# Kernel tuning notes

Measured on AMD Instinct MI355X. Metric: run time of the kernel, lower is better.

Reference implementation:

```python
import jax, jax.numpy as jnp
import numpy as np

EPS = 1e-5

def _ln(x, g, b):
    mu = x.mean(-1, keepdims=True)
    var = ((x - mu) ** 2).mean(-1, keepdims=True)
    return (x - mu) * jax.lax.rsqrt(var + EPS) * g + b

def setup_inputs() -> dict:
    B, K, D, H, T = 64, 64, 128, 128, 4
    key = jax.random.key(0)
    ks = jax.random.split(key, 20)
    s = 0.02
    inp = {
        "slots": jax.random.normal(ks[0], (B, K, D), jnp.float32),
        "edge_probs": jax.random.uniform(ks[1], (B, K, K), jnp.float32),
        "edge_types": jax.random.uniform(ks[2], (B, K, K, T), jnp.float32),
        # f_self: LayerNorm(D) -> Linear(D,H) -> ReLU -> Linear(H,D)
        "ls_g": jnp.ones((D,), jnp.float32),
        "ls_b": jnp.zeros((D,), jnp.float32),
        "ws1": jax.random.normal(ks[3], (D, H), jnp.float32) * s,
        "bs1": jnp.zeros((H,), jnp.float32),
        "ws2": jax.random.normal(ks[4], (H, D), jnp.float32) * s,
        "bs2": jnp.zeros((D,), jnp.float32),
        # f_inter[tau]: Linear(2D,H) -> ReLU -> Linear(H,H) -> ReLU -> Linear(H,D), stacked over T
        "wi1": jax.random.normal(ks[5], (T, 2 * D, H), jnp.float32) * s,
        "bi1": jnp.zeros((T, H), jnp.float32),
        "wi2": jax.random.normal(ks[6], (T, H, H), jnp.float32) * s,
        "bi2": jnp.zeros((T, H), jnp.float32),
        "wi3": jax.random.normal(ks[7], (T, H, D), jnp.float32) * s,
        "bi3": jnp.zeros((T, D), jnp.float32),
        # update_mlp: LayerNorm(2D) -> Linear(2D,H) -> ReLU -> Linear(H,D)
        "lu_g": jnp.ones((2 * D,), jnp.float32),
        "lu_b": jnp.zeros((2 * D,), jnp.float32),
        "wu1": jax.random.normal(ks[8], (2 * D, H), jnp.float32) * s,
        "bu1": jnp.zeros((H,), jnp.float32),
        "wu2": jax.random.normal(ks[9], (H, D), jnp.float32) * s,
        "bu2": jnp.zeros((D,), jnp.float32),
    }
    return inp

NUM_MP = 2

def reference(slots, edge_probs, edge_types, ls_g, ls_b, ws1, bs1, ws2, bs2,
              wi1, bi1, wi2, bi2, wi3, bi3, lu_g, lu_b, wu1, bu1, wu2, bu2):
    B, K, D = slots.shape
    T = edge_types.shape[-1]
    h = slots
    for _ in range(NUM_MP):
        # f_self
        delta_self = jax.nn.relu(_ln(h, ls_g, ls_b) @ ws1 + bs1) @ ws2 + bs2
        # all-pairs features: cat[b,i,j] = [h[b,i] (sender), h[b,j] (receiver)]
        sender = jnp.broadcast_to(h[:, :, None, :], (B, K, K, D))
        receiver = jnp.broadcast_to(h[:, None, :, :], (B, K, K, D))
        pair = jnp.concatenate([sender, receiver], axis=-1)  # [B,K,K,2D]
        delta_inter = jnp.zeros_like(h)
        for tau in range(T):
            x = jax.nn.relu(pair @ wi1[tau] + bi1[tau])
            x = jax.nn.relu(x @ wi2[tau] + bi2[tau])
            eff = x @ wi3[tau] + bi3[tau]  # [B,K,K,D]
            w = edge_probs[..., None] * edge_types[..., tau, None]  # [B,K,K,1]
            delta_inter = delta_inter + (eff * w).sum(axis=1)  # sum over sender i
        combined = jnp.concatenate([h + delta_self, delta_inter], axis=-1)
        update = jax.nn.relu(_ln(combined, lu_g, lu_b) @ wu1 + bu1) @ wu2 + bu2
        h = h + update  # residual=True
    return h
```

## Files before the change

### kernel.cpp

```cpp
#include <hip/hip_runtime.h>
#include <hip/hip_fp16.h>

#define BATCH 64
#define KSLOT 64
#define DDIM  128
#define HDIM  128
#define TTYPE 4
#define NSLOT (BATCH*KSLOT)
#define EPSLN 1e-5f
#define YROW  544

typedef _Float16 v8h __attribute__((ext_vector_type(8)));
typedef _Float16 v4h __attribute__((ext_vector_type(4)));
typedef _Float16 v2h __attribute__((ext_vector_type(2)));
typedef __fp16   v2y __attribute__((ext_vector_type(2)));
typedef float    v4f __attribute__((ext_vector_type(4)));

__device__ __forceinline__ float waveAllSum(float v) {
    #pragma unroll
    for (int m = 1; m < 64; m <<= 1) v += __shfl_xor(v, m, 64);
    return v;
}

__global__ __launch_bounds__(256) void k_wconv(
        const float* __restrict__ ws1, const float* __restrict__ wi1,
        const float* __restrict__ ws2, const float* __restrict__ wu1,
        const float* __restrict__ wu2, const float* __restrict__ wi3,
        const float* __restrict__ wi2, const float* __restrict__ bi1,
        const float* __restrict__ bi3,
        const float* __restrict__ ep, const float* __restrict__ et,
        __half* __restrict__ ws1T, __half* __restrict__ wi1catT,
        __half* __restrict__ ws2T, __half* __restrict__ wu1T,
        __half* __restrict__ wu2T, __half* __restrict__ w3catT,
        __half* __restrict__ w2T16, float* __restrict__ biascat,
        __half* __restrict__ wPre) {
    __shared__ __align__(16) float tile[128*132];
    int bx = blockIdx.x, tid = threadIdx.x;
    if (bx >= 22) {
        int bx2 = bx - 22, tau = bx2 & 3, b = bx2 >> 2;
        const float* epb = ep + (size_t)b*4096;
        const float* etb = et + (size_t)b*4096*TTYPE + tau;
        __half* dst = wPre + ((size_t)tau*BATCH + b)*4096;
        for (int idx = tid; idx < 4096; idx += 256)
            dst[idx] = __float2half(epb[idx] * etb[(size_t)idx*TTYPE]);
        return;
    }
    if (bx == 21) {
        for (int idx = tid; idx < 128*32; idx += 256) {
            int o = idx >> 5, c = idx & 31;
            w3catT[(size_t)o*YROW + 512 + c] = (c < 4) ? __float2half(bi3[c*DDIM + o]) : __float2half(0.f);
        }
        for (int idx = tid; idx < 1024; idx += 256) {
            int th = idx >> 7, o = idx & 127;
            biascat[idx] = (th & 1) ? bi1[(th>>1)*HDIM + o] : 0.f;
        }
        return;
    }
    const float* src; __half* dst; int dstride = 128, dcol = 0;
    if (bx == 0)      { src = ws1; dst = ws1T; }
    else if (bx <= 8) { int th = bx-1, tau = th>>1, half = th&1;
                        src = wi1 + ((size_t)tau*256 + half*128)*128;
                        dst = wi1catT + (size_t)th*128*128; }
    else if (bx == 9) { src = ws2; dst = ws2T; }
    else if (bx ==10) { src = wu2; dst = wu2T; }
    else if (bx <=12) { int hh = bx-11; src = wu1 + (size_t)hh*128*128;
                        dst = wu1T; dstride = 256; dcol = hh*128; }
    else if (bx <=16) { int tau = bx-13; src = wi3 + (size_t)tau*16384;
                        dst = w3catT; dstride = YROW; dcol = tau*128; }
    else              { int tau = bx-17; src = wi2 + (size_t)tau*16384;
                        dst = w2T16 + (size_t)tau*16384; }
    for (int idx = tid; idx < 4096; idx += 256) {
        int r = idx >> 5, c4 = idx & 31;
        *(float4*)&tile[r*132 + c4*4] = *(const float4*)&src[(size_t)r*128 + c4*4];
    }
    __syncthreads();
    for (int idx = tid; idx < 8192; idx += 256) {
        int n = idx >> 6, kp = idx & 63;
        __half2 p = __floats2half2_rn(tile[(2*kp)*132 + n], tile[(2*kp+1)*132 + n]);
        *(__half2*)&dst[(size_t)n*dstride + dcol + 2*kp] = p;
    }
}

__global__ __launch_bounds__(256) void k_front(
        const float* __restrict__ h,
        const __half* __restrict__ wi1catT, const float* __restrict__ biascat,
        const float* __restrict__ ls_g, const float* __restrict__ ls_b,
        const __half* __restrict__ ws1T, const float* __restrict__ bs1,
        const __half* __restrict__ ws2T, const float* __restrict__ bs2,
        __half* __restrict__ AtCt, float* __restrict__ comb128) {
    __shared__ __align__(16) char smem[17152];
    int tid = threadIdx.x, lane = tid & 63, w = tid >> 6;
    int n = lane & 15, quad = lane >> 4;
    int row0 = blockIdx.x*16, nb = blockIdx.y;
    if (nb < 4) {
        _Float16* Ha = (_Float16*)smem;
        v8h bfrag[4][4];
        #pragma unroll
        for (int ot = 0; ot < 4; ot++) {
            int col = nb*256 + w*64 + ot*16 + n;
            #pragma unroll
            for (int ks = 0; ks < 4; ks++)
                bfrag[ot][ks] = *(const v8h*)&wi1catT[(size_t)col*128 + ks*32 + quad*8];
        }
        for (int u = tid; u < 16*32; u += 256) {
            int r = u >> 5, c4 = (u & 31)*4;
            float4 f = *(const float4*)&h[(size_t)(row0 + r)*128 + c4];
            *(__half2*)&Ha[r*136 + c4]     = __floats2half2_rn(f.x, f.y);
            *(__half2*)&Ha[r*136 + c4 + 2] = __floats2half2_rn(f.z, f.w);
        }
        __syncthreads();
        v4f acc[4];
        #pragma unroll
        for (int ot = 0; ot < 4; ot++) {
            float b0 = biascat[nb*256 + w*64 + ot*16 + n];
            acc[ot] = (v4f){b0, b0, b0, b0};
        }
        #pragma unroll
        for (int ks = 0; ks < 4; ks++) {
            v8h a = *(const v8h*)&Ha[n*136 + ks*32 + quad*8];
            #pragma unroll
            for (int ot = 0; ot < 4; ot++)
                acc[ot] = __builtin_amdgcn_mfma_f32_16x16x32_f16(a, bfrag[ot][ks], acc[ot], 0, 0, 0);
        }
        __syncthreads();
        _Float16* Ot = (_Float16*)smem;
        #pragma unroll
        for (int ot = 0; ot < 4; ot++)
            #pragma unroll
            for (int r = 0; r < 4; r++)
                Ot[(quad*4 + r)*264 + w*64 + ot*16 + n] = (_Float16)acc[ot][r];
        __syncthreads();
        #pragma unroll
        for (int u = 0; u < 2; u++) {
            int k = tid + u*256;
            int r = k >> 5, c8 = (k & 31)*8;
            *(v8h*)&AtCt[(size_t)(row0 + r)*1024 + nb*256 + c8] = *(const v8h*)&Ot[r*264 + c8];
        }
    } else {
        float*    Hrow = (float*)smem;
        _Float16* Xa = (_Float16*)(smem + 8448);
        _Float16* Tt = (_Float16*)(smem + 8448 + 4352);
        v8h b1[2][4], b2[2][4];
        #pragma unroll
        for (int ot = 0; ot < 2; ot++) {
            int col = w*32 + ot*16 + n;
            #pragma unroll
            for (int ks = 0; ks < 4; ks++) {
                b1[ot][ks] = *(const v8h*)&ws1T[(size_t)col*128 + ks*32 + quad*8];
                b2[ot][ks] = *(const v8h*)&ws2T[(size_t)col*128 + ks*32 + quad*8];
            }
        }
        for (int u = tid; u < 16*32; u += 256) {
            int r = u >> 5, c4 = (u & 31)*4;
            *(float4*)&Hrow[r*132 + c4] = *(const float4*)&h[(size_t)(row0 + r)*128 + c4];
        }
        __syncthreads();
        #pragma unroll
        for (int rr = 0; rr < 4; rr++) {
            int r = w*4 + rr;
            float x0 = Hrow[r*132 + 2*lane], x1 = Hrow[r*132 + 2*lane + 1];
            float mu = waveAllSum(x0 + x1) * (1.f/128.f);
            float d0 = x0 - mu, d1 = x1 - mu;
            float var = waveAllSum(d0*d0 + d1*d1) * (1.f/128.f);
            float rs = rsqrtf(var + EPSLN);
            float2 gv = *(const float2*)&ls_g[2*lane];
            float2 bv = *(const float2*)&ls_b[2*lane];
            *(__half2*)&Xa[r*136 + 2*lane] = __floats2half2_rn(d0*rs*gv.x + bv.x, d1*rs*gv.y + bv.y);
        }
        __syncthreads();
        v4f acc[2];
        #pragma unroll
        for (int ot = 0; ot < 2; ot++) { float b0 = bs1[w*32 + ot*16 + n]; acc[ot] = (v4f){b0,b0,b0,b0}; }
        #pragma unroll
        for (int ks = 0; ks < 4; ks++) {
            v8h a = *(const v8h*)&Xa[n*136 + ks*32 + quad*8];
            #pragma unroll
            for (int ot = 0; ot < 2; ot++)
                acc[ot] = __builtin_amdgcn_mfma_f32_16x16x32_f16(a, b1[ot][ks], acc[ot], 0, 0, 0);
        }
        #pragma unroll
        for (int ot = 0; ot < 2; ot++)
            #pragma unroll
            for (int r = 0; r < 4; r++)
                Tt[(quad*4 + r)*136 + w*32 + ot*16 + n] = (_Float16)fmaxf(acc[ot][r], 0.f);
        __syncthreads();
        #pragma unroll
        for (int ot = 0; ot < 2; ot++) { float b0 = bs2[w*32 + ot*16 + n]; acc[ot] = (v4f){b0,b0,b0,b0}; }
        #pragma unroll
        for (int ks = 0; ks < 4; ks++) {
            v8h a = *(const v8h*)&Tt[n*136 + ks*32 + quad*8];
            #pragma unroll
            for (int ot = 0; ot < 2; ot++)
                acc[ot] = __builtin_amdgcn_mfma_f32_16x16x32_f16(a, b2[ot][ks], acc[ot], 0, 0, 0);
        }
        #pragma unroll
        for (int ot = 0; ot < 2; ot++)
            #pragma unroll
            for (int r = 0; r < 4; r++) {
                int rr = quad*4 + r, col = w*32 + ot*16 + n;
                comb128[(size_t)(row0 + rr)*128 + col] = Hrow[rr*132 + col] + acc[ot][r];
            }
    }
}

#define LROW 136
__global__ __launch_bounds__(512) void k_pair(
        const __half* __restrict__ AtCt,
        const __half* __restrict__ w2T16,
        const float* __restrict__ bi2,
        const __half* __restrict__ wPre,
        __half* __restrict__ Ycat) {
    __shared__ __align__(16) _Float16 w2T[HDIM*LROW];
    __shared__ __align__(16) _Float16 Cs[KSLOT*LROW];
    __shared__ __align__(16) _Float16 As[KSLOT*LROW];
    __shared__ __align__(16) _Float16 wS[KSLOT*KSLOT];
    int bx = blockIdx.x, b = bx >> 2, tau = bx & 3;
    int tid = threadIdx.x, lane = tid & 63, w = tid >> 6;
    int jt = w >> 1, oh = w & 1, quad = lane >> 4, n = lane & 15;

    for (int idx = tid; idx < 2048; idx += 512) {
        int o = idx >> 4, seg = (idx & 15)*8;
        *(v8h*)&w2T[o*LROW + seg] = *(const v8h*)&w2T16[((size_t)tau*128 + o)*128 + seg];
    }
    for (int u = tid; u < 1024; u += 512) {
        int j = u >> 4, seg = (u & 15)*8;
        const __half* rp = AtCt + (size_t)(b*KSLOT + j)*1024 + tau*256 + seg;
        *(v8h*)&As[j*LROW + seg] = *(const v8h*)&rp[0];
        *(v8h*)&Cs[j*LROW + seg] = *(const v8h*)&rp[128];
    }
    {
        const __half* wsrc = wPre + ((size_t)tau*BATCH + b)*4096;
        int base = tid*8;
        *(v8h*)&wS[base] = *(const v8h*)&wsrc[base];
    }
    __syncthreads();

    v8h bfrag[4][4];
    #pragma unroll
    for (int ot = 0; ot < 4; ot++)
        #pragma unroll
        for (int ks = 0; ks < 4; ks++)
            bfrag[ot][ks] = *(const v8h*)&w2T[(oh*64 + ot*16 + n)*LROW + ks*32 + quad*8];
    v8h cfrag[4];
    #pragma unroll
    for (int ks = 0; ks < 4; ks++)
        cfrag[ks] = *(const v8h*)&Cs[(jt*16 + n)*LROW + ks*32 + quad*8];
    v4f biasvec[4];
    #pragma unroll
    for (int ot = 0; ot < 4; ot++) {
        float b0 = bi2[tau*HDIM + oh*64 + ot*16 + n];
        biasvec[ot] = (v4f){b0, b0, b0, b0};
    }

    v4h yacch[4];
    #pragma unroll
    for (int ot = 0; ot < 4; ot++) yacch[ot] = (v4h){0,0,0,0};
    v4h wsacch = (v4h){0,0,0,0};
    const v8h zero8 = {0,0,0,0,0,0,0,0};
    const v4h zero4h = {0,0,0,0};

    v8h aN[4]; v4h wvN;
    #pragma unroll
    for (int ks = 0; ks < 4; ks++) aN[ks] = *(const v8h*)&As[ks*32 + quad*8];
    wvN = *(const v4h*)&wS[jt*16 + quad*4];

    for (int i = 0; i < KSLOT; ++i) {
        v8h a[4]; v4h wv = wvN;
        #pragma unroll
        for (int ks = 0; ks < 4; ks++) a[ks] = aN[ks];
        if (i < KSLOT-1) {
            #pragma unroll
            for (int ks = 0; ks < 4; ks++)
                aN[ks] = *(const v8h*)&As[(i+1)*LROW + ks*32 + quad*8];
            wvN = *(const v4h*)&wS[(i+1)*KSLOT + jt*16 + quad*4];
        }
        v8h x1[4];
        #pragma unroll
        for (int ks = 0; ks < 4; ks++)
            x1[ks] = __builtin_elementwise_max(a[ks] + cfrag[ks], zero8);
        #pragma unroll
        for (int ot = 0; ot < 4; ot++) {
            v4f acc = __builtin_amdgcn_mfma_f32_16x16x32_f16(x1[0], bfrag[ot][0], biasvec[ot], 0, 0, 0);
            #pragma unroll
            for (int ks = 1; ks < 4; ks++)
                acc = __builtin_amdgcn_mfma_f32_16x16x32_f16(x1[ks], bfrag[ot][ks], acc, 0, 0, 0);
            v2h lo = __builtin_bit_cast(v2h, __builtin_amdgcn_cvt_pkrtz(acc[0], acc[1]));
            v2h hi = __builtin_bit_cast(v2h, __builtin_amdgcn_cvt_pkrtz(acc[2], acc[3]));
            v4h rel = {lo[0], lo[1], hi[0], hi[1]};
            rel = __builtin_elementwise_max(rel, zero4h);
            yacch[ot] = yacch[ot] + wv * rel;
        }
        wsacch = wsacch + wv;
    }

    #pragma unroll
    for (int r = 0; r < 4; r++) {
        int j = jt*16 + quad*4 + r;
        __half* yb = Ycat + (size_t)(b*KSLOT + j)*YROW + tau*128 + oh*64;
        #pragma unroll
        for (int ot = 0; ot < 4; ot++)
            yb[ot*16 + n] = __float2half((float)yacch[ot][r]);
    }
    if (oh == 0 && n == 0) {
        #pragma unroll
        for (int r = 0; r < 4; r++)
            Ycat[(size_t)(b*KSLOT + jt*16 + quad*4 + r)*YROW + 512 + tau] = __float2half((float)wsacch[r]);
    }
}

__global__ __launch_bounds__(512, 2) void k_mega(
        const __half* __restrict__ Ycat, const __half* __restrict__ w3catT,
        const float* __restrict__ comb128,
        const float* __restrict__ g, const float* __restrict__ bb,
        const __half* __restrict__ wu1T, const float* __restrict__ bu1,
        const __half* __restrict__ wu2T, const float* __restrict__ bu2,
        const float* __restrict__ h, float* __restrict__ hout) {
    __shared__ __align__(16) _Float16 Ys[16*552];
    __shared__ __align__(16) float    Crow[16*260];
    __shared__ __align__(16) _Float16 Xa[16*264];
    __shared__ __align__(16) _Float16 Ut[16*136];
    int tid = threadIdx.x, lane = tid & 63, w = tid >> 6;
    int n = lane & 15, quad = lane >> 4;
    int row0 = blockIdx.x*16;
    v8h f3[17];
    #pragma unroll
    for (int ks = 0; ks < 17; ks++)
        f3[ks] = *(const v8h*)&w3catT[(size_t)(w*16 + n)*YROW + ks*32 + quad*8];
    v8h f1[8];
    #pragma unroll
    for (int ks = 0; ks < 8; ks++)
        f1[ks] = *(const v8h*)&wu1T[(size_t)(w*16 + n)*256 + ks*32 + quad*8];
    v8h f2[4];
    #pragma unroll
    for (int ks = 0; ks < 4; ks++)
        f2[ks] = *(const v8h*)&wu2T[(size_t)(w*16 + n)*128 + ks*32 + quad*8];

    for (int u = tid; u < 1024; u += 512) {
        int r = u >> 6, seg = (u & 63)*8;
        *(v8h*)&Ys[r*552 + seg] = *(const v8h*)&Ycat[(size_t)(row0 + r)*YROW + seg];
    }
    if (tid < 64) {
        int r = tid >> 2, seg = 512 + (tid & 3)*8;
        *(v8h*)&Ys[r*552 + seg] = *(const v8h*)&Ycat[(size_t)(row0 + r)*YROW + seg];
    }
    {
        int r = tid >> 5, c4 = (tid & 31)*4;
        *(float4*)&Crow[r*260 + c4] = *(const float4*)&comb128[(size_t)(row0 + r)*128 + c4];
    }
    __syncthreads();
    {
        v4f acc = (v4f){0.f,0.f,0.f,0.f};
        #pragma unroll
        for (int ks = 0; ks < 17; ks++) {
            v8h a = *(const v8h*)&Ys[n*552 + ks*32 + quad*8];
            acc = __builtin_amdgcn_mfma_f32_16x16x32_f16(a, f3[ks], acc, 0, 0, 0);
        }
        #pragma unroll
        for (int r = 0; r < 4; r++)
            Crow[(quad*4 + r)*260 + 128 + w*16 + n] = acc[r];
    }
    __syncthreads();
    #pragma unroll
    for (int rr = 0; rr < 2; rr++) {
        int r = w*2 + rr;
        float4 v = *(const float4*)&Crow[r*260 + 4*lane];
        float mu = waveAllSum(v.x + v.y + v.z + v.w) * (1.f/256.f);
        float d0 = v.x-mu, d1 = v.y-mu, d2 = v.z-mu, d3 = v.w-mu;
        float var = waveAllSum(d0*d0 + d1*d1 + d2*d2 + d3*d3) * (1.f/256.f);
        float rs = rsqrtf(var + EPSLN);
        float4 gv = *(const float4*)&g[4*lane];
        float4 bv = *(const float4*)&bb[4*lane];
        *(__half2*)&Xa[r*264 + 4*lane]     = __floats2half2_rn(d0*rs*gv.x + bv.x, d1*rs*gv.y + bv.y);
        *(__half2*)&Xa[r*264 + 4*lane + 2] = __floats2half2_rn(d2*rs*gv.z + bv.z, d3*rs*gv.w + bv.w);
    }
    __syncthreads();
    {
        float b0 = bu1[w*16 + n];
        v4f acc = (v4f){b0, b0, b0, b0};
        #pragma unroll
        for (int ks = 0; ks < 8; ks++) {
            v8h a = *(const v8h*)&Xa[n*264 + ks*32 + quad*8];
            acc = __builtin_amdgcn_mfma_f32_16x16x32_f16(a, f1[ks], acc, 0, 0, 0);
        }
        #pragma unroll
        for (int r = 0; r < 4; r++)
            Ut[(quad*4 + r)*136 + w*16 + n] = (_Float16)fmaxf(acc[r], 0.f);
    }
    __syncthreads();
    {
        float b0 = bu2[w*16 + n];
        v4f acc = (v4f){b0, b0, b0, b0};
        #pragma unroll
        for (int ks = 0; ks < 4; ks++) {
            v8h a = *(const v8h*)&Ut[n*136 + ks*32 + quad*8];
            acc = __builtin_amdgcn_mfma_f32_16x16x32_f16(a, f2[ks], acc, 0, 0, 0);
        }
        #pragma unroll
        for (int r = 0; r < 4; r++) {
            int rr = quad*4 + r, col = w*16 + n;
            hout[(size_t)(row0 + rr)*128 + col] = h[(size_t)(row0 + rr)*128 + col] + acc[r];
        }
    }
}

extern "C" void kernel_launch(void* const* d_in, const int* in_sizes, int n_in,
                              void* d_out, int out_size, void* d_ws, size_t ws_size,
                              hipStream_t stream) {
    const float* slots = (const float*)d_in[0];
    const float* ep    = (const float*)d_in[1];
    const float* et    = (const float*)d_in[2];
    const float* ls_g  = (const float*)d_in[3];
    const float* ls_b  = (const float*)d_in[4];
    const float* ws1   = (const float*)d_in[5];
    const float* bs1   = (const float*)d_in[6];
    const float* ws2   = (const float*)d_in[7];
    const float* bs2   = (const float*)d_in[8];
    const float* wi1   = (const float*)d_in[9];
    const float* bi1   = (const float*)d_in[10];
    const float* wi2   = (const float*)d_in[11];
    const float* bi2   = (const float*)d_in[12];
    const float* wi3   = (const float*)d_in[13];
    const float* bi3   = (const float*)d_in[14];
    const float* lu_g  = (const float*)d_in[15];
    const float* lu_b  = (const float*)d_in[16];
    const float* wu1   = (const float*)d_in[17];
    const float* bu1   = (const float*)d_in[18];
    const float* wu2   = (const float*)d_in[19];
    const float* bu2   = (const float*)d_in[20];
    float* out = (float*)d_out;

    char* p = (char*)d_ws;
    float*  h_buf   = (float*)p;   p += (size_t)NSLOT*DDIM*4;
    __half* AtCt    = (__half*)p;  p += (size_t)NSLOT*1024*2;
    __half* Ycat    = (__half*)p;  p += (size_t)NSLOT*YROW*2;
    float*  comb128 = (float*)p;   p += (size_t)NSLOT*128*4;
    __half* wPre    = (__half*)p;  p += (size_t)TTYPE*BATCH*4096*2;
    __half* ws1T    = (__half*)p;  p += 128*128*2;
    __half* wi1catT = (__half*)p;  p += 1024*128*2;
    __half* ws2T    = (__half*)p;  p += 128*128*2;
    __half* wu1T    = (__half*)p;  p += 128*256*2;
    __half* wu2T    = (__half*)p;  p += 128*128*2;
    __half* w3catT  = (__half*)p;  p += 128*YROW*2;
    __half* w2T16   = (__half*)p;  p += 4*128*128*2;
    float*  biascat = (float*)p;   p += 1024*4;

    k_wconv<<<22 + 256, 256, 0, stream>>>(ws1, wi1, ws2, wu1, wu2, wi3, wi2, bi1, bi3,
                                          ep, et, ws1T, wi1catT, ws2T, wu1T, wu2T,
                                          w3catT, w2T16, biascat, wPre);

    for (int mp = 0; mp < 2; mp++) {
        const float* h = (mp == 0) ? slots : h_buf;
        float* hout = (mp == 0) ? h_buf : out;
        k_front<<<dim3(256, 5), 256, 0, stream>>>(h, wi1catT, biascat, ls_g, ls_b,
                                                  ws1T, bs1, ws2T, bs2, AtCt, comb128);
        k_pair<<<BATCH*TTYPE, 512, 0, stream>>>(AtCt, w2T16, bi2, wPre, Ycat);
        k_mega<<<NSLOT/16, 512, 0, stream>>>(Ycat, w3catT, comb128, lu_g, lu_b,
                                             wu1T, bu1, wu2T, bu2, h, hout);
    }
}
```

Baseline: 219.6 us.

## Fuse first interaction-layer GEMM into pair kernel, drop AtCt intermediate

Moves the per-type sender/receiver projection (h @ wi1 halves) out of the front kernel and computes it inside k_pair from h loaded directly into shared memory. This removes the 16 MB fp16 AtCt global write and read round trip. The self-MLP becomes its own kernel, k_self. In exchange k_pair gains an extra GEMM stage, 17 KB more shared memory, and B-fragments read straight from global memory, which may lower occupancy and lengthen the critical path.

```diff
diff --git a/kernel.cpp b/kernel.cpp
--- a/kernel.cpp
+++ b/kernel.cpp
@@ -13,7 +13,6 @@
 typedef _Float16 v8h __attribute__((ext_vector_type(8)));
 typedef _Float16 v4h __attribute__((ext_vector_type(4)));
 typedef _Float16 v2h __attribute__((ext_vector_type(2)));
-typedef __fp16   v2y __attribute__((ext_vector_type(2)));
 typedef float    v4f __attribute__((ext_vector_type(4)));
 
 __device__ __forceinline__ float waveAllSum(float v) {
@@ -81,131 +80,85 @@
     }
 }
 
-__global__ __launch_bounds__(256) void k_front(
+__global__ __launch_bounds__(256) void k_self(
         const float* __restrict__ h,
-        const __half* __restrict__ wi1catT, const float* __restrict__ biascat,
         const float* __restrict__ ls_g, const float* __restrict__ ls_b,
         const __half* __restrict__ ws1T, const float* __restrict__ bs1,
         const __half* __restrict__ ws2T, const float* __restrict__ bs2,
-        __half* __restrict__ AtCt, float* __restrict__ comb128) {
-    __shared__ __align__(16) char smem[17152];
+        float* __restrict__ comb128) {
+    __shared__ __align__(16) float    Hrow[16*132];
+    __shared__ __align__(16) _Float16 Xa[16*136];
+    __shared__ __align__(16) _Float16 Tt[16*136];
     int tid = threadIdx.x, lane = tid & 63, w = tid >> 6;
     int n = lane & 15, quad = lane >> 4;
-    int row0 = blockIdx.x*16, nb = blockIdx.y;
-    if (nb < 4) {
-        _Float16* Ha = (_Float16*)smem;
-        v8h bfrag[4][4];
-        #pragma unroll
-        for (int ot = 0; ot < 4; ot++) {
-            int col = nb*256 + w*64 + ot*16 + n;
-            #pragma unroll
-            for (int ks = 0; ks < 4; ks++)
-                bfrag[ot][ks] = *(const v8h*)&wi1catT[(size_t)col*128 + ks*32 + quad*8];
-        }
-        for (int u = tid; u < 16*32; u += 256) {
-            int r = u >> 5, c4 = (u & 31)*4;
-            float4 f = *(const float4*)&h[(size_t)(row0 + r)*128 + c4];
-            *(__half2*)&Ha[r*136 + c4]     = __floats2half2_rn(f.x, f.y);
-            *(__half2*)&Ha[r*136 + c4 + 2] = __floats2half2_rn(f.z, f.w);
-        }
-        __syncthreads();
-        v4f acc[4];
-        #pragma unroll
-        for (int ot = 0; ot < 4; ot++) {
-            float b0 = biascat[nb*256 + w*64 + ot*16 + n];
-            acc[ot] = (v4f){b0, b0, b0, b0};
-        }
+    int row0 = blockIdx.x*16;
+    v8h b1[2][4], b2[2][4];
+    #pragma unroll
+    for (int ot = 0; ot < 2; ot++) {
+        int col = w*32 + ot*16 + n;
         #pragma unroll
         for (int ks = 0; ks < 4; ks++) {
-            v8h a = *(const v8h*)&Ha[n*136 + ks*32 + quad*8];
-            #pragma unroll
-            for (int ot = 0; ot < 4; ot++)
-                acc[ot] = __builtin_amdgcn_mfma_f32_16x16x32_f16(a, bfrag[ot][ks], acc[ot], 0, 0, 0);
-        }
-        __syncthreads();
-        _Float16* Ot = (_Float16*)smem;
-        #pragma unroll
-        for (int ot = 0; ot < 4; ot++)
-            #pragma unroll
-            for (int r = 0; r < 4; r++)
-                Ot[(quad*4 + r)*264 + w*64 + ot*16 + n] = (_Float16)acc[ot][r];
-        __syncthreads();
-        #pragma unroll
-        for (int u = 0; u < 2; u++) {
-            int k = tid + u*256;
-            int r = k >> 5, c8 = (k & 31)*8;
-            *(v8h*)&AtCt[(size_t)(row0 + r)*1024 + nb*256 + c8] = *(const v8h*)&Ot[r*264 + c8];
-        }
-    } else {
-        float*    Hrow = (float*)smem;
-        _Float16* Xa = (_Float16*)(smem + 8448);
-        _Float16* Tt = (_Float16*)(smem + 8448 + 4352);
-        v8h b1[2][4], b2[2][4];
-        #pragma unroll
-        for (int ot = 0; ot < 2; ot++) {
-            int col = w*32 + ot*16 + n;
-            #pragma unroll
-            for (int ks = 0; ks < 4; ks++) {
-                b1[ot][ks] = *(const v8h*)&ws1T[(size_t)col*128 + ks*32 + quad*8];
-                b2[ot][ks] = *(const v8h*)&ws2T[(size_t)col*128 + ks*32 + quad*8];
-            }
-        }
-        for (int u = tid; u < 16*32; u += 256) {
-            int r = u >> 5, c4 = (u & 31)*4;
-            *(float4*)&Hrow[r*132 + c4] = *(const float4*)&h[(size_t)(row0 + r)*128 + c4];
-        }
-        __syncthreads();
-        #pragma unroll
-        for (int rr = 0; rr < 4; rr++) {
-            int r = w*4 + rr;
-            float x0 = Hrow[r*132 + 2*lane], x1 = Hrow[r*132 + 2*lane + 1];
-            float mu = waveAllSum(x0 + x1) * (1.f/128.f);
-            float d0 = x0 - mu, d1 = x1 - mu;
-            float var = waveAllSum(d0*d0 + d1*d1) * (1.f/128.f);
-            float rs = rsqrtf(var + EPSLN);
-            float2 gv = *(const float2*)&ls_g[2*lane];
-            float2 bv = *(const float2*)&ls_b[2*lane];
-            *(__half2*)&Xa[r*136 + 2*lane] = __floats2half2_rn(d0*rs*gv.x + bv.x, d1*rs*gv.y + bv.y);
-        }
-        __syncthreads();
-        v4f acc[2];
-        #pragma unroll
-        for (int ot = 0; ot < 2; ot++) { float b0 = bs1[w*32 + ot*16 + n]; acc[ot] = (v4f){b0,b0,b0,b0}; }
-        #pragma unroll
-        for (int ks = 0; ks < 4; ks++) {
-            v8h a = *(const v8h*)&Xa[n*136 + ks*32 + quad*8];
-            #pragma unroll
-            for (int ot = 0; ot < 2; ot++)
-                acc[ot] = __builtin_amdgcn_mfma_f32_16x16x32_f16(a, b1[ot][ks], acc[ot], 0, 0, 0);
-        }
+            b1[ot][ks] = *(const v8h*)&ws1T[(size_t)col*128 + ks*32 + quad*8];
+            b2[ot][ks] = *(const v8h*)&ws2T[(size_t)col*128 + ks*32 + quad*8];
+        }
+    }
+    for (int u = tid; u < 16*32; u += 256) {
+        int r = u >> 5, c4 = (u & 31)*4;
+        *(float4*)&Hrow[r*132 + c4] = *(const float4*)&h[(size_t)(row0 + r)*128 + c4];
+    }
+    __syncthreads();
+    #pragma unroll
+    for (int rr = 0; rr < 4; rr++) {
+        int r = w*4 + rr;
+        float x0 = Hrow[r*132 + 2*lane], x1 = Hrow[r*132 + 2*lane + 1];
+        float mu = waveAllSum(x0 + x1) * (1.f/128.f);
+        float d0 = x0 - mu, d1 = x1 - mu;
+        float var = waveAllSum(d0*d0 + d1*d1) * (1.f/128.f);
+        float rs = rsqrtf(var + EPSLN);
+        float2 gv = *(const float2*)&ls_g[2*lane];
+        float2 bv = *(const float2*)&ls_b[2*lane];
+        *(__half2*)&Xa[r*136 + 2*lane] = __floats2half2_rn(d0*rs*gv.x + bv.x, d1*rs*gv.y + bv.y);
+    }
+    __syncthreads();
+    v4f acc[2];
+    #pragma unroll
+    for (int ot = 0; ot < 2; ot++) { float b0 = bs1[w*32 + ot*16 + n]; acc[ot] = (v4f){b0,b0,b0,b0}; }
+    #pragma unroll
+    for (int ks = 0; ks < 4; ks++) {
+        v8h a = *(const v8h*)&Xa[n*136 + ks*32 + quad*8];
         #pragma unroll
         for (int ot = 0; ot < 2; ot++)
-            #pragma unroll
-            for (int r = 0; r < 4; r++)
-                Tt[(quad*4 + r)*136 + w*32 + ot*16 + n] = (_Float16)fmaxf(acc[ot][r], 0.f);
-        __syncthreads();
-        #pragma unroll
-        for (int ot = 0; ot < 2; ot++) { float b0 = bs2[w*32 + ot*16 + n]; acc[ot] = (v4f){b0,b0,b0,b0}; }
-        #pragma unroll
-        for (int ks = 0; ks < 4; ks++) {
-            v8h a = *(const v8h*)&Tt[n*136 + ks*32 + quad*8];
-            #pragma unroll
-            for (int ot = 0; ot < 2; ot++)
-                acc[ot] = __builtin_amdgcn_mfma_f32_16x16x32_f16(a, b2[ot][ks], acc[ot], 0, 0, 0);
-        }
+            acc[ot] = __builtin_amdgcn_mfma_f32_16x16x32_f16(a, b1[ot][ks], acc[ot], 0, 0, 0);
+    }
+    #pragma unroll
+    for (int ot = 0; ot < 2; ot++)
+        #pragma unroll
+        for (int r = 0; r < 4; r++)
+            Tt[(quad*4 + r)*136 + w*32 + ot*16 + n] = (_Float16)fmaxf(acc[ot][r], 0.f);
+    __syncthreads();
+    #pragma unroll
+    for (int ot = 0; ot < 2; ot++) { float b0 = bs2[w*32 + ot*16 + n]; acc[ot] = (v4f){b0,b0,b0,b0}; }
+    #pragma unroll
+    for (int ks = 0; ks < 4; ks++) {
+        v8h a = *(const v8h*)&Tt[n*136 + ks*32 + quad*8];
         #pragma unroll
         for (int ot = 0; ot < 2; ot++)
-            #pragma unroll
-            for (int r = 0; r < 4; r++) {
-                int rr = quad*4 + r, col = w*32 + ot*16 + n;
-                comb128[(size_t)(row0 + rr)*128 + col] = Hrow[rr*132 + col] + acc[ot][r];
-            }
-    }
+            acc[ot] = __builtin_amdgcn_mfma_f32_16x16x32_f16(a, b2[ot][ks], acc[ot], 0, 0, 0);
+    }
+    #pragma unroll
+    for (int ot = 0; ot < 2; ot++)
+        #pragma unroll
+        for (int r = 0; r < 4; r++) {
+            int rr = quad*4 + r, col = w*32 + ot*16 + n;
+            comb128[(size_t)(row0 + rr)*128 + col] = Hrow[rr*132 + col] + acc[ot][r];
+        }
 }
 
 #define LROW 136
 __global__ __launch_bounds__(512) void k_pair(
-        const __half* __restrict__ AtCt,
+        const float* __restrict__ h,
+        const __half* __restrict__ wi1catT,
+        const float* __restrict__ biascat,
         const __half* __restrict__ w2T16,
         const float* __restrict__ bi2,
         const __half* __restrict__ wPre,
@@ -214,6 +167,7 @@
     __shared__ __align__(16) _Float16 Cs[KSLOT*LROW];
     __shared__ __align__(16) _Float16 As[KSLOT*LROW];
     __shared__ __align__(16) _Float16 wS[KSLOT*KSLOT];
+    __shared__ __align__(16) _Float16 hs[KSLOT*136];
     int bx = blockIdx.x, b = bx >> 2, tau = bx & 3;
     int tid = threadIdx.x, lane = tid & 63, w = tid >> 6;
     int jt = w >> 1, oh = w & 1, quad = lane >> 4, n = lane & 15;
@@ -222,16 +176,43 @@
         int o = idx >> 4, seg = (idx & 15)*8;
         *(v8h*)&w2T[o*LROW + seg] = *(const v8h*)&w2T16[((size_t)tau*128 + o)*128 + seg];
     }
-    for (int u = tid; u < 1024; u += 512) {
-        int j = u >> 4, seg = (u & 15)*8;
-        const __half* rp = AtCt + (size_t)(b*KSLOT + j)*1024 + tau*256 + seg;
-        *(v8h*)&As[j*LROW + seg] = *(const v8h*)&rp[0];
-        *(v8h*)&Cs[j*LROW + seg] = *(const v8h*)&rp[128];
-    }
-    {
-        const __half* wsrc = wPre + ((size_t)tau*BATCH + b)*4096;
+    {
+        int row = tid >> 3, c0 = (tid & 7)*16;
+        const float* hp = &h[(size_t)(b*KSLOT + row)*128 + c0];
+        #pragma unroll
+        for (int q = 0; q < 4; q++) {
+            float4 f = *(const float4*)&hp[q*4];
+            *(__half2*)&hs[row*136 + c0 + q*4]     = __floats2half2_rn(f.x, f.y);
+            *(__half2*)&hs[row*136 + c0 + q*4 + 2] = __floats2half2_rn(f.z, f.w);
+        }
+    }
+    {
         int base = tid*8;
-        *(v8h*)&wS[base] = *(const v8h*)&wsrc[base];
+        *(v8h*)&wS[base] = *(const v8h*)&wPre[((size_t)tau*BATCH + b)*4096 + base];
+    }
+    __syncthreads();
+
+    {
+        int hf = w >> 2, rt = w & 3;
+        const __half* wb = wi1catT + (size_t)(tau*2 + hf)*128*128;
+        const float* bcp = biascat + (tau*2 + hf)*128;
+        _Float16* dst = hf ? Cs : As;
+        v8h afr[4];
+        #pragma unroll
+        for (int ks = 0; ks < 4; ks++)
+            afr[ks] = *(const v8h*)&hs[(rt*16 + n)*136 + ks*32 + quad*8];
+        #pragma unroll
+        for (int ot = 0; ot < 8; ot++) {
+            float b0 = bcp[ot*16 + n];
+            v4f acc = (v4f){b0, b0, b0, b0};
+            #pragma unroll
+            for (int ks = 0; ks < 4; ks++)
+                acc = __builtin_amdgcn_mfma_f32_16x16x32_f16(
+                    afr[ks], *(const v8h*)&wb[(size_t)(ot*16 + n)*128 + ks*32 + quad*8], acc, 0, 0, 0);
+            #pragma unroll
+            for (int r = 0; r < 4; r++)
+                dst[(rt*16 + quad*4 + r)*LROW + ot*16 + n] = (_Float16)acc[r];
+        }
     }
     __syncthreads();
 
@@ -431,7 +412,6 @@
 
     char* p = (char*)d_ws;
     float*  h_buf   = (float*)p;   p += (size_t)NSLOT*DDIM*4;
-    __half* AtCt    = (__half*)p;  p += (size_t)NSLOT*1024*2;
     __half* Ycat    = (__half*)p;  p += (size_t)NSLOT*YROW*2;
     float*  comb128 = (float*)p;   p += (size_t)NSLOT*128*4;
     __half* wPre    = (__half*)p;  p += (size_t)TTYPE*BATCH*4096*2;
@@ -451,9 +431,8 @@
     for (int mp = 0; mp < 2; mp++) {
         const float* h = (mp == 0) ? slots : h_buf;
         float* hout = (mp == 0) ? h_buf : out;
-        k_front<<<dim3(256, 5), 256, 0, stream>>>(h, wi1catT, biascat, ls_g, ls_b,
-                                                  ws1T, bs1, ws2T, bs2, AtCt, comb128);
-        k_pair<<<BATCH*TTYPE, 512, 0, stream>>>(AtCt, w2T16, bi2, wPre, Ycat);
+        k_self<<<NSLOT/16, 256, 0, stream>>>(h, ls_g, ls_b, ws1T, bs1, ws2T, bs2, comb128);
+        k_pair<<<BATCH*TTYPE, 512, 0, stream>>>(h, wi1catT, biascat, w2T16, bi2, wPre, Ycat);
         k_mega<<<NSLOT/16, 512, 0, stream>>>(Ycat, w3catT, comb128, lu_g, lu_b,
                                              wu1T, bu1, wu2T, bu2, h, hout);
     }
```

Result: faster. 210.9 us (-4.0%).
